# Kernel optimization log

Measured on AMD Instinct MI355X. Metric: run time of the kernel, lower is better.

The kernel has to match this reference:

```python
import jax, jax.numpy as jnp
import numpy as np

# dims: B=32 batch, F=40 max_frames, NB=36 num_boxes, R=512 region size, H=512 hidden
# feat_size D = R + 2H = 1536 ; relation attn input = 2D = 3072

def _soft_attention(feats, hidden, Wf, bf, Wh, bh, wa):
    # feats: (N, L, Din), hidden: (N, H) -> att feat (N, Din), alpha (N, L)
    e = jnp.tanh(feats @ Wf.T + bf + (hidden @ Wh.T + bh)[:, None, :]) @ wa  # (N, L)
    alpha = jax.nn.softmax(e, axis=1)
    att = jnp.einsum('nl,nld->nd', alpha, feats)
    return att, alpha


def setup_inputs() -> dict:
    key = jax.random.key(0)
    ks = jax.random.split(key, 16)
    B, F, NB, R, H = 32, 40, 36, 512, 512
    D = R + 2 * H  # 1536
    s = 0.02
    inp = {
        'i3d_feats': jax.random.normal(ks[0], (B, F, 2 * H), jnp.float32),
        'object_feats': jax.random.normal(ks[1], (B, F, NB, R), jnp.float32),
        'hidden_state': jax.random.normal(ks[2], (B, H), jnp.float32),
        # spatial SoftAttention(R, H, H)
        'Ws_f': jax.random.normal(ks[3], (H, R), jnp.float32) * s,
        'bs_f': jnp.zeros((H,), jnp.float32),
        'Ws_h': jax.random.normal(ks[4], (H, H), jnp.float32) * s,
        'bs_h': jnp.zeros((H,), jnp.float32),
        'was': jax.random.normal(ks[5], (H,), jnp.float32) * s,
        # relation SoftAttention(2D, H, H)
        'Wr_f': jax.random.normal(ks[6], (H, 2 * D), jnp.float32) * s,
        'br_f': jnp.zeros((H,), jnp.float32),
        'Wr_h': jax.random.normal(ks[7], (H, H), jnp.float32) * s,
        'br_h': jnp.zeros((H,), jnp.float32),
        'war': jax.random.normal(ks[8], (H,), jnp.float32) * s,
    }
    return inp


def reference(i3d_feats, object_feats, hidden_state,
              Ws_f, bs_f, Ws_h, bs_h, was,
              Wr_f, br_f, Wr_h, br_h, war):
    B, F, NB, R = object_feats.shape
    # ---- spatial attention over boxes (per frame) ----
    feats = object_feats.reshape(B * F, NB, R)
    hidden_rep = jnp.repeat(hidden_state, F, axis=0)  # == hidden.repeat(1,F).reshape(B*F,-1)
    obj_att, _ = _soft_attention(feats, hidden_rep, Ws_f, bs_f, Ws_h, bs_h, was)
    obj_att = obj_att.reshape(B, F, R)
    feat = jnp.concatenate([obj_att, i3d_feats], axis=-1)  # (B, F, D)
    D = feat.shape[-1]
    # ---- relation attention over all F*F frame pairs ----
    # pairwise[b, i*F + j] = concat(feat[b, j], feat[b, i])  (feat1 varies fast, feat2 slow)
    # Decompose Wr_f @ concat(fj, fi) = Wr1 @ fj + Wr2 @ fi to avoid O(F^2 * 2D) tensor.
    Wr1, Wr2 = Wr_f[:, :D], Wr_f[:, D:]
    p1 = feat @ Wr1.T  # (B, F, H), applied to fast index j
    p2 = feat @ Wr2.T  # (B, F, H), applied to slow index i
    hproj = hidden_state @ Wr_h.T + br_h  # (B, H)
    e = jnp.tanh(p2[:, :, None, :] + p1[:, None, :, :] + (hproj + br_f)[:, None, None, :]) @ war  # (B,F,F) [i,j]
    alpha = jax.nn.softmax(e.reshape(B, F * F), axis=1).reshape(B, F, F)
    # weighted sum of concat(feat[j], feat[i]) splits into two marginal sums
    rel1 = jnp.einsum('bij,bjd->bd', alpha, feat)
    rel2 = jnp.einsum('bij,bid->bd', alpha, feat)
    return jnp.concatenate([rel1, rel2], axis=-1)  # (B, 2D)
```

## Files before the change

kernel.cpp:

```cpp
#include <hip/hip_runtime.h>
#include <stdint.h>

#define B_SZ 32
#define F_SZ 40
#define NB_SZ 36
#define R_SZ 512
#define H_SZ 512
#define D_SZ 1536
#define M1 (B_SZ * F_SZ * NB_SZ)
#define NROW (B_SZ * F_SZ)
#define FNB (F_SZ * NB_SZ)

typedef __attribute__((ext_vector_type(8))) short short8;
typedef __attribute__((ext_vector_type(4))) float f32x4;

__device__ __forceinline__ unsigned short f2bf(float f) {
    unsigned int x = __float_as_uint(f);
    return (unsigned short)((x + 0x7fffu + ((x >> 16) & 1u)) >> 16);
}
__device__ __forceinline__ float bf2f(unsigned short u) {
    union { unsigned int i; float f; } v; v.i = ((unsigned int)u) << 16; return v.f;
}
__device__ __forceinline__ unsigned int cvtpk(float lo, float hi) {
    unsigned int r;
    asm("v_cvt_pk_bf16_f32 %0, %1, %2" : "=v"(r) : "v"(lo), "v"(hi));
    return r;
}
__device__ __forceinline__ float fast_rcp(float x) {
    float r; asm("v_rcp_f32 %0, %1" : "=v"(r) : "v"(x)); return r;
}
__device__ __forceinline__ float fast_tanh(float x) {
    float t = __builtin_amdgcn_exp2f(2.8853900817779268f * x);
    return 1.0f - 2.0f * fast_rcp(t + 1.0f);
}

__device__ __forceinline__ void gload_lds16(const void* gsrc, void* ldst) {
    __builtin_amdgcn_global_load_lds(
        (const __attribute__((address_space(1))) unsigned int*)gsrc,
        (__attribute__((address_space(3))) unsigned int*)ldst, 16, 0, 0);
}

__global__ __launch_bounds__(256) void k_pre(
    const float* __restrict__ hidden,
    const float* __restrict__ Wsh, const float* __restrict__ bsh,
    const float* __restrict__ bsf,
    const float* __restrict__ Wrh, const float* __restrict__ brh,
    const float* __restrict__ brf,
    float* __restrict__ hs, float* __restrict__ hr,
    const float* __restrict__ Wsf, unsigned short* __restrict__ Wsb)
{
    const int t = threadIdx.x;
    if (blockIdx.x >= 256) {
        int i = ((blockIdx.x - 256) * 256 + t) * 8;
        float4 f0 = *(const float4*)(Wsf + i);
        float4 f1 = *(const float4*)(Wsf + i + 4);
        uint4 pk = {cvtpk(f0.x, f0.y), cvtpk(f0.z, f0.w),
                    cvtpk(f1.x, f1.y), cvtpk(f1.z, f1.w)};
        *(uint4*)(Wsb + i) = pk;
        return;
    }
    __shared__ float hid[H_SZ];
    const int b = blockIdx.x >> 3, hc = blockIdx.x & 7;
    for (int i = t; i < H_SZ; i += 256) hid[i] = hidden[b * H_SZ + i];
    __syncthreads();
    const int h = hc * 64 + (t >> 2), kq = t & 3;
    const float* r1 = Wsh + (size_t)h * H_SZ + kq * 128;
    const float* r2 = Wrh + (size_t)h * H_SZ + kq * 128;
    const float* hh = hid + kq * 128;
    float a1 = 0.f, a2 = 0.f;
    for (int k = 0; k < 128; k += 4) {
        float4 v1 = *(const float4*)(r1 + k);
        float4 v2 = *(const float4*)(r2 + k);
        a1 += hh[k] * v1.x + hh[k+1] * v1.y + hh[k+2] * v1.z + hh[k+3] * v1.w;
        a2 += hh[k] * v2.x + hh[k+1] * v2.y + hh[k+2] * v2.z + hh[k+3] * v2.w;
    }
    a1 += __shfl_xor(a1, 1); a1 += __shfl_xor(a1, 2);
    a2 += __shfl_xor(a2, 1); a2 += __shfl_xor(a2, 2);
    if (kq == 0) {
        hs[b * H_SZ + h] = a1 + bsh[h] + bsf[h];
        hr[b * H_SZ + h] = a2 + brh[h] + brf[h];
    }
}

__global__ __launch_bounds__(256, 3) void k_e1_mfma(
    const float* __restrict__ feats,
    const unsigned short* __restrict__ Wsb,
    const float* __restrict__ was,
    const float* __restrict__ hs,
    float* __restrict__ e1p)
{
    __shared__ __align__(16) unsigned char As[2][64 * 128];
    __shared__ __align__(16) unsigned char Bs[2][128 * 128];
    __shared__ float hsl[2][256];
    __shared__ float wasl[256];
    __shared__ float eps[2][64];

    const int bx = blockIdx.x;
    const int wid = (bx & 7) * 180 + (bx >> 3);
    const int mb = wid >> 1, by = wid & 1;
    const int m0 = mb * 64, hb = by * 256;
    const int t = threadIdx.x;
    const int b0 = m0 / FNB, b1 = (m0 + 63) / FNB;
    const int thr = (b0 + 1) * FNB - m0;

    hsl[0][t] = hs[b0 * H_SZ + hb + t];
    hsl[1][t] = hs[b1 * H_SZ + hb + t];
    wasl[t]   = was[hb + t];

    const int lane = t & 63, w = t >> 6;
    const int wr = w >> 1, wc = w & 1;
    const int l15 = lane & 15, lk = lane >> 4;

    int ar[2], brw[4];
#pragma unroll
    for (int i = 0; i < 2; i++) ar[i] = wr * 32 + i * 16 + l15;
#pragma unroll
    for (int j = 0; j < 4; j++) brw[j] = wc * 64 + j * 16 + l15;

    const int srow = t >> 3;
    const int scol = t & 7;
    const int wub  = (t & 192) * 16;

    float4 alo[2], ahi[2];
    f32x4 acc[2][8] = {};
    float ep[2][4] = {{0.f}};

#define E1_LOAD_A(K0) do { \
    _Pragma("unroll") \
    for (int it = 0; it < 2; it++) { \
        int cid = it * 256 + t; \
        int r = cid >> 3, c = cid & 7; \
        const float* src = feats + (size_t)(m0 + r) * R_SZ + (K0) + c * 8; \
        alo[it] = *(const float4*)src; \
        ahi[it] = *(const float4*)(src + 4); \
    } } while (0)

#define E1_WRITE_A(AB) do { \
    _Pragma("unroll") \
    for (int it = 0; it < 2; it++) { \
        int cid = it * 256 + t; \
        int r = cid >> 3, c = cid & 7; \
        uint4 pk = {cvtpk(alo[it].x, alo[it].y), cvtpk(alo[it].z, alo[it].w), \
                    cvtpk(ahi[it].x, ahi[it].y), cvtpk(ahi[it].z, ahi[it].w)}; \
        *(uint4*)(&As[AB][r * 128 + ((c ^ (r & 7)) << 4)]) = pk; \
    } } while (0)

#define E1_STAGE_B(BUF, HP, K0) do { \
    _Pragma("unroll") \
    for (int it = 0; it < 4; it++) { \
        int r = it * 32 + srow; \
        int gc = scol ^ (r & 7); \
        gload_lds16(Wsb + (size_t)(hb + (HP) * 128 + r) * R_SZ + (K0) + gc * 8, \
                    &Bs[BUF][it * 4096 + wub]); \
    } } while (0)

#define E1_COMPUTE(HP, BB, AB) do { \
    __builtin_amdgcn_s_setprio(1); \
    _Pragma("unroll") \
    for (int ks = 0; ks < 2; ks++) { \
        short8 a[2], bv[4]; \
        int c = ks * 4 + lk; \
        _Pragma("unroll") \
        for (int i = 0; i < 2; i++) \
            a[i] = *(const short8*)(&As[AB][ar[i] * 128 + ((c ^ (ar[i] & 7)) << 4)]); \
        _Pragma("unroll") \
        for (int j = 0; j < 4; j++) \
            bv[j] = *(const short8*)(&Bs[BB][brw[j] * 128 + ((c ^ (brw[j] & 7)) << 4)]); \
        _Pragma("unroll") \
        for (int i = 0; i < 2; i++) \
        _Pragma("unroll") \
        for (int j = 0; j < 4; j++) \
            acc[i][(HP) * 4 + j] = __builtin_amdgcn_mfma_f32_16x16x32_bf16( \
                a[i], bv[j], acc[i][(HP) * 4 + j], 0, 0, 0); \
    } \
    __builtin_amdgcn_s_setprio(0); \
    } while (0)

    E1_LOAD_A(0);
    E1_STAGE_B(0, 0, 0);
    E1_WRITE_A(0);
    asm volatile("s_waitcnt vmcnt(0) lgkmcnt(0)\ns_barrier" ::: "memory");

#pragma unroll
    for (int ki = 0; ki < 8; ki++) {
        const int ab = ki & 1;
        E1_STAGE_B(1, 1, ki * 64);
        if (ki < 7) E1_LOAD_A((ki + 1) * 64);
        E1_COMPUTE(0, 0, ab);
        if (ki < 7) {
            asm volatile("s_waitcnt vmcnt(4)\ns_barrier" ::: "memory");
        } else {
            asm volatile("s_waitcnt vmcnt(0)\ns_barrier" ::: "memory");
        }
        if (ki < 7) E1_STAGE_B(0, 0, (ki + 1) * 64);
        E1_COMPUTE(1, 1, ab);
        if (ki < 7) E1_WRITE_A(ab ^ 1);
        asm volatile("s_waitcnt vmcnt(0) lgkmcnt(0)\ns_barrier" ::: "memory");
    }

#pragma unroll
    for (int jj = 0; jj < 8; jj++) {
        int hl = (jj >> 2) * 128 + wc * 64 + (jj & 3) * 16 + l15;
        float wv = wasl[hl];
#pragma unroll
        for (int i = 0; i < 2; i++) {
#pragma unroll
            for (int q = 0; q < 4; q++) {
                int r = wr * 32 + i * 16 + lk * 4 + q;
                float hv = hsl[r >= thr ? 1 : 0][hl];
                ep[i][q] += fast_tanh(acc[i][jj][q] + hv) * wv;
            }
        }
    }
#pragma unroll
    for (int i = 0; i < 2; i++)
#pragma unroll
        for (int q = 0; q < 4; q++) {
            float v = ep[i][q];
            v += __shfl_xor(v, 1);
            v += __shfl_xor(v, 2);
            v += __shfl_xor(v, 4);
            v += __shfl_xor(v, 8);
            if (l15 == 0) eps[wc][wr * 32 + i * 16 + lk * 4 + q] = v;
        }
    __syncthreads();
    if (t < 64) e1p[(size_t)by * M1 + m0 + t] = eps[0][t] + eps[1][t];
#undef E1_LOAD_A
#undef E1_WRITE_A
#undef E1_STAGE_B
#undef E1_COMPUTE
}

__global__ __launch_bounds__(256) void k_softatt(
    const float* __restrict__ feats,
    const float* __restrict__ i3d,
    const float* __restrict__ e1p,
    unsigned short* __restrict__ feat)
{
    __shared__ float alpha[2][NB_SZ];
    const int n0 = blockIdx.x * 2;
    const int t = threadIdx.x;
    const int w = t >> 6;

    if (w < 2) {
        const int n = n0 + w, lane = t & 63;
        float v = -1e30f;
        if (lane < NB_SZ) {
            int idx = n * NB_SZ + lane;
            v = e1p[idx] + e1p[M1 + idx];
        }
        float m = v;
#pragma unroll
        for (int off = 32; off; off >>= 1) m = fmaxf(m, __shfl_xor(m, off));
        float ex = (lane < NB_SZ) ? __expf(v - m) : 0.f;
        float ssum = ex;
#pragma unroll
        for (int off = 32; off; off >>= 1) ssum += __shfl_xor(ssum, off);
        if (lane < NB_SZ) alpha[w][lane] = ex / ssum;
    }
    __syncthreads();

    const int g = t >> 7, lc = t & 127;
    const int n = n0 + g;
    float4 a4 = {0.f, 0.f, 0.f, 0.f};
    const float* base = feats + (size_t)n * NB_SZ * R_SZ + lc * 4;
    for (int ll = 0; ll < NB_SZ; ll++) {
        float al = alpha[g][ll];
        float4 pv = *(const float4*)(base + ll * R_SZ);
        a4.x += al * pv.x; a4.y += al * pv.y;
        a4.z += al * pv.z; a4.w += al * pv.w;
    }
    uint2 att = {cvtpk(a4.x, a4.y), cvtpk(a4.z, a4.w)};
    *(uint2*)(feat + (size_t)n * D_SZ + lc * 4) = att;

    const float* ib = i3d + (size_t)n * 1024 + lc * 8;
    float4 iv0 = *(const float4*)ib;
    float4 iv1 = *(const float4*)(ib + 4);
    uint4 pk = {cvtpk(iv0.x, iv0.y), cvtpk(iv0.z, iv0.w),
                cvtpk(iv1.x, iv1.y), cvtpk(iv1.z, iv1.w)};
    *(uint4*)(feat + (size_t)n * D_SZ + 512 + lc * 8) = pk;
}

__global__ __launch_bounds__(256) void k_pgemm_mfma(
    const unsigned short* __restrict__ feat,
    const float* __restrict__ Wrf,
    float* __restrict__ p)
{
    __shared__ __align__(16) unsigned char As[2][64 * 256];
    __shared__ __align__(16) unsigned char Bs[2][32 * 256];

    const int bx = blockIdx.x;
    const int wid = (bx & 7) * 80 + (bx >> 3);
    const int mb = wid % 20, nb = wid / 20;
    const int m0 = mb * 64, j0 = nb * 32;
    const int t = threadIdx.x;

    const int lane = t & 63, w = t >> 6;
    const int wrm = w >> 1, wcn = w & 1;
    const int l15 = lane & 15, lk = lane >> 4;

    int arow[2];
    arow[0] = wrm * 32 + l15; arow[1] = arow[0] + 16;
    const int brow = wcn * 16 + l15;

    const size_t brow_base = (j0 < 512) ? (size_t)j0 * 3072
                                        : ((size_t)(j0 - 512) * 3072 + 1536);

    float4 blo[2], bhi[2];
    f32x4 acc[2] = {};

#define PG_STAGE_A(BUF, K0) do { \
    _Pragma("unroll") \
    for (int it = 0; it < 4; it++) { \
        int cid = it * 256 + t; \
        int r = cid >> 4, c = cid & 15; \
        int gc = c ^ (r & 7); \
        gload_lds16(feat + (size_t)(m0 + r) * D_SZ + (K0) + gc * 8, \
                    &As[BUF][it * 4096 + (t & 192) * 16]); \
    } } while (0)

#define PG_LOAD_B(K0) do { \
    _Pragma("unroll") \
    for (int it = 0; it < 2; it++) { \
        int cid = it * 256 + t; \
        int r = cid >> 4, c = cid & 15; \
        const float* src = Wrf + brow_base + (size_t)r * 3072 + (K0) + c * 8; \
        blo[it] = *(const float4*)src; \
        bhi[it] = *(const float4*)(src + 4); \
    } } while (0)

#define PG_WRITE_B(BUF) do { \
    _Pragma("unroll") \
    for (int it = 0; it < 2; it++) { \
        int cid = it * 256 + t; \
        int r = cid >> 4, c = cid & 15; \
        uint4 pk = {cvtpk(blo[it].x, blo[it].y), cvtpk(blo[it].z, blo[it].w), \
                    cvtpk(bhi[it].x, bhi[it].y), cvtpk(bhi[it].z, bhi[it].w)}; \
        *(uint4*)(&Bs[BUF][r * 256 + ((c ^ (r & 7)) << 4)]) = pk; \
    } } while (0)

#define PG_COMPUTE(BUF) do { \
    __builtin_amdgcn_s_setprio(1); \
    _Pragma("unroll") \
    for (int ks = 0; ks < 4; ks++) { \
        int c = ks * 4 + lk; \
        short8 a0 = *(const short8*)(&As[BUF][arow[0] * 256 + ((c ^ (arow[0] & 7)) << 4)]); \
        short8 a1 = *(const short8*)(&As[BUF][arow[1] * 256 + ((c ^ (arow[1] & 7)) << 4)]); \
        short8 bv = *(const short8*)(&Bs[BUF][brow * 256 + ((c ^ (brow & 7)) << 4)]); \
        acc[0] = __builtin_amdgcn_mfma_f32_16x16x32_bf16(a0, bv, acc[0], 0, 0, 0); \
        acc[1] = __builtin_amdgcn_mfma_f32_16x16x32_bf16(a1, bv, acc[1], 0, 0, 0); \
    } \
    __builtin_amdgcn_s_setprio(0); \
    } while (0)

    PG_LOAD_B(0);
    PG_STAGE_A(0, 0);
    PG_WRITE_B(0);
    __syncthreads();

#pragma unroll
    for (int ki = 0; ki < 12; ki++) {
        const int cur = ki & 1;
        if (ki < 11) {
            PG_LOAD_B((ki + 1) * 128);
            PG_STAGE_A(cur ^ 1, (ki + 1) * 128);
        }
        PG_COMPUTE(cur);
        if (ki < 11) PG_WRITE_B(cur ^ 1);
        __syncthreads();
    }

#pragma unroll
    for (int i = 0; i < 2; i++)
#pragma unroll
        for (int q = 0; q < 4; q++) {
            int row = m0 + wrm * 32 + i * 16 + lk * 4 + q;
            int col = j0 + wcn * 16 + l15;
            p[(size_t)row * 1024 + col] = acc[i][q];
        }
#undef PG_STAGE_A
#undef PG_LOAD_B
#undef PG_WRITE_B
#undef PG_COMPUTE
}

__global__ __launch_bounds__(256) void k_e2(
    const float* __restrict__ p,
    const float* __restrict__ hr,
    const float* __restrict__ war,
    float* __restrict__ e2)
{
    __shared__ float p1l[F_SZ][512];
    const int blk = blockIdx.x;
    const int b = blk / 10, io = blk % 10;
    const int t = threadIdx.x;
    const int w = t >> 6, l = t & 63;

#pragma unroll
    for (int u = 0; u < 10; u++) {
        int cid = u * 256 + t;
        int r = cid >> 6, c = cid & 63;
        const float* src = p + (size_t)(b * F_SZ + r) * 1024 + c * 8;
        *(float4*)&p1l[r][c * 8]     = *(const float4*)src;
        *(float4*)&p1l[r][c * 8 + 4] = *(const float4*)(src + 4);
    }

    const int i = io * 4 + w;
    const int ni = b * F_SZ + i;
    float base[8], warf[8];
    {
        float4 pa = *(const float4*)(p + (size_t)ni * 1024 + 512 + l * 8);
        float4 pb = *(const float4*)(p + (size_t)ni * 1024 + 512 + l * 8 + 4);
        float4 ha = *(const float4*)(hr + b * H_SZ + l * 8);
        float4 hb = *(const float4*)(hr + b * H_SZ + l * 8 + 4);
        base[0] = pa.x + ha.x; base[1] = pa.y + ha.y; base[2] = pa.z + ha.z; base[3] = pa.w + ha.w;
        base[4] = pb.x + hb.x; base[5] = pb.y + hb.y; base[6] = pb.z + hb.z; base[7] = pb.w + hb.w;
        float4 wa = *(const float4*)(war + l * 8);
        float4 wb = *(const float4*)(war + l * 8 + 4);
        warf[0] = wa.x; warf[1] = wa.y; warf[2] = wa.z; warf[3] = wa.w;
        warf[4] = wb.x; warf[5] = wb.y; warf[6] = wb.z; warf[7] = wb.w;
    }
    __syncthreads();

    for (int j = 0; j < F_SZ; j++) {
        const float* r = p1l[j];
        float4 va = *(const float4*)(r + l * 8);
        float4 vb = *(const float4*)(r + l * 8 + 4);
        float pv[8] = {va.x, va.y, va.z, va.w, vb.x, vb.y, vb.z, vb.w};
        float s = 0.f;
#pragma unroll
        for (int u = 0; u < 8; u++) s += fast_tanh(pv[u] + base[u]) * warf[u];
#pragma unroll
        for (int off = 32; off; off >>= 1) s += __shfl_xor(s, off);
        if (l == 0) e2[(size_t)b * 1600 + i * F_SZ + j] = s;
    }
}

__global__ __launch_bounds__(256) void k_out(
    const float* __restrict__ e2,
    const unsigned short* __restrict__ feat,
    float* __restrict__ out)
{
    __shared__ float alpha[1600];
    __shared__ float red[4];
    __shared__ float rs[F_SZ], cs[F_SZ];
    const int b = blockIdx.x / 6, sx = blockIdx.x % 6;
    const int t = threadIdx.x;
    const int w = t >> 6, l = t & 63;

    float lm = -1e30f;
    for (int idx = t; idx < 1600; idx += 256) {
        float v = e2[(size_t)b * 1600 + idx];
        alpha[idx] = v;
        lm = fmaxf(lm, v);
    }
#pragma unroll
    for (int off = 32; off; off >>= 1) lm = fmaxf(lm, __shfl_xor(lm, off));
    if (l == 0) red[w] = lm;
    __syncthreads();
    float M = fmaxf(fmaxf(red[0], red[1]), fmaxf(red[2], red[3]));
    __syncthreads();
    float ls = 0.f;
    for (int idx = t; idx < 1600; idx += 256) {
        float ex = __expf(alpha[idx] - M);
        alpha[idx] = ex;
        ls += ex;
    }
#pragma unroll
    for (int off = 32; off; off >>= 1) ls += __shfl_xor(ls, off);
    if (l == 0) red[w] = ls;
    __syncthreads();
    float inv = 1.f / (red[0] + red[1] + red[2] + red[3]);

    if (t < F_SZ) {
        float s = 0.f;
        for (int j = 0; j < F_SZ; j++) s += alpha[t * F_SZ + j];
        rs[t] = s * inv;
    } else if (t >= 128 && t < 128 + F_SZ) {
        int j = t - 128;
        float s = 0.f;
        for (int i2 = 0; i2 < F_SZ; i2++) s += alpha[i2 * F_SZ + j];
        cs[j] = s * inv;
    }
    __syncthreads();

    const int cb = sx * 256;
    float a1 = 0.f, a2 = 0.f;
    for (int r = 0; r < F_SZ; r++) {
        float w1 = cs[r], w2 = rs[r];
        float f = bf2f(feat[(size_t)(b * F_SZ + r) * D_SZ + cb + t]);
        a1 += w1 * f;
        a2 += w2 * f;
    }
    out[(size_t)b * 3072 + cb + t]        = a1;
    out[(size_t)b * 3072 + 1536 + cb + t] = a2;
}

extern "C" void kernel_launch(void* const* d_in, const int* in_sizes, int n_in,
                              void* d_out, int out_size, void* d_ws, size_t ws_size,
                              hipStream_t stream) {
    const float* i3d    = (const float*)d_in[0];
    const float* objf   = (const float*)d_in[1];
    const float* hidden = (const float*)d_in[2];
    const float* Wsf    = (const float*)d_in[3];
    const float* bsf    = (const float*)d_in[4];
    const float* Wsh    = (const float*)d_in[5];
    const float* bsh    = (const float*)d_in[6];
    const float* was    = (const float*)d_in[7];
    const float* Wrf    = (const float*)d_in[8];
    const float* brf    = (const float*)d_in[9];
    const float* Wrh    = (const float*)d_in[10];
    const float* brh    = (const float*)d_in[11];
    const float* war    = (const float*)d_in[12];
    float* out = (float*)d_out;

    char* ws = (char*)d_ws;
    float* hs  = (float*)(ws);
    float* hr  = (float*)(ws + 65536);
    float* p   = (float*)(ws + 131072);
    float* e1p = (float*)(ws + 131072);
    unsigned short* Wsb = (unsigned short*)(ws + 4849664);
    float* e2  = (float*)(ws + 5373952);
    unsigned short* feat = (unsigned short*)(ws + 5578752);

    k_pre<<<dim3(384), dim3(256), 0, stream>>>(hidden, Wsh, bsh, bsf, Wrh, brh, brf, hs, hr, Wsf, Wsb);
    k_e1_mfma<<<dim3(1440), dim3(256), 0, stream>>>(objf, Wsb, was, hs, e1p);
    k_softatt<<<dim3(640), dim3(256), 0, stream>>>(objf, i3d, e1p, feat);
    k_pgemm_mfma<<<dim3(640), dim3(256), 0, stream>>>(feat, Wrf, p);
    k_e2<<<dim3(320), dim3(256), 0, stream>>>(p, hr, war, e2);
    k_out<<<dim3(192), dim3(256), 0, stream>>>(e2, feat, out);
}
```

Measured before the change: 262.9 us.

## Split e1 launch in two, drop setprio and custom waitcnt barriers, reshape e2

```diff
diff --git a/kernel.cpp b/kernel.cpp
--- a/kernel.cpp
+++ b/kernel.cpp
@@ -87,7 +87,8 @@
     const unsigned short* __restrict__ Wsb,
     const float* __restrict__ was,
     const float* __restrict__ hs,
-    float* __restrict__ e1p)
+    float* __restrict__ e1p,
+    int wbase)
 {
     __shared__ __align__(16) unsigned char As[2][64 * 128];
     __shared__ __align__(16) unsigned char Bs[2][128 * 128];
@@ -96,7 +97,7 @@
     __shared__ float eps[2][64];
 
     const int bx = blockIdx.x;
-    const int wid = (bx & 7) * 180 + (bx >> 3);
+    const int wid = wbase + (bx & 7) * 90 + (bx >> 3);
     const int mb = wid >> 1, by = wid & 1;
     const int m0 = mb * 64, hb = by * 256;
     const int t = threadIdx.x;
@@ -155,7 +156,6 @@
     } } while (0)
 
 #define E1_COMPUTE(HP, BB, AB) do { \
-    __builtin_amdgcn_s_setprio(1); \
     _Pragma("unroll") \
     for (int ks = 0; ks < 2; ks++) { \
         short8 a[2], bv[4]; \
@@ -172,30 +172,23 @@
         for (int j = 0; j < 4; j++) \
             acc[i][(HP) * 4 + j] = __builtin_amdgcn_mfma_f32_16x16x32_bf16( \
                 a[i], bv[j], acc[i][(HP) * 4 + j], 0, 0, 0); \
-    } \
-    __builtin_amdgcn_s_setprio(0); \
-    } while (0)
+    } } while (0)
 
     E1_LOAD_A(0);
     E1_STAGE_B(0, 0, 0);
     E1_WRITE_A(0);
-    asm volatile("s_waitcnt vmcnt(0) lgkmcnt(0)\ns_barrier" ::: "memory");
-
-#pragma unroll
+    __syncthreads();
+
     for (int ki = 0; ki < 8; ki++) {
         const int ab = ki & 1;
         E1_STAGE_B(1, 1, ki * 64);
         if (ki < 7) E1_LOAD_A((ki + 1) * 64);
         E1_COMPUTE(0, 0, ab);
-        if (ki < 7) {
-            asm volatile("s_waitcnt vmcnt(4)\ns_barrier" ::: "memory");
-        } else {
-            asm volatile("s_waitcnt vmcnt(0)\ns_barrier" ::: "memory");
-        }
+        __syncthreads();
         if (ki < 7) E1_STAGE_B(0, 0, (ki + 1) * 64);
         E1_COMPUTE(1, 1, ab);
         if (ki < 7) E1_WRITE_A(ab ^ 1);
-        asm volatile("s_waitcnt vmcnt(0) lgkmcnt(0)\ns_barrier" ::: "memory");
+        __syncthreads();
     }
 
 #pragma unroll
@@ -340,7 +333,6 @@
     } } while (0)
 
 #define PG_COMPUTE(BUF) do { \
-    __builtin_amdgcn_s_setprio(1); \
     _Pragma("unroll") \
     for (int ks = 0; ks < 4; ks++) { \
         int c = ks * 4 + lk; \
@@ -349,9 +341,7 @@
         short8 bv = *(const short8*)(&Bs[BUF][brow * 256 + ((c ^ (brow & 7)) << 4)]); \
         acc[0] = __builtin_amdgcn_mfma_f32_16x16x32_bf16(a0, bv, acc[0], 0, 0, 0); \
         acc[1] = __builtin_amdgcn_mfma_f32_16x16x32_bf16(a1, bv, acc[1], 0, 0, 0); \
-    } \
-    __builtin_amdgcn_s_setprio(0); \
-    } while (0)
+    } } while (0)
 
     PG_LOAD_B(0);
     PG_STAGE_A(0, 0);
@@ -384,28 +374,27 @@
 #undef PG_COMPUTE
 }
 
-__global__ __launch_bounds__(256) void k_e2(
+__global__ __launch_bounds__(320) void k_e2(
     const float* __restrict__ p,
     const float* __restrict__ hr,
     const float* __restrict__ war,
     float* __restrict__ e2)
 {
     __shared__ float p1l[F_SZ][512];
-    const int blk = blockIdx.x;
-    const int b = blk / 10, io = blk % 10;
+    const int b = blockIdx.x >> 3, io = blockIdx.x & 7;
     const int t = threadIdx.x;
     const int w = t >> 6, l = t & 63;
 
 #pragma unroll
-    for (int u = 0; u < 10; u++) {
-        int cid = u * 256 + t;
+    for (int u = 0; u < 8; u++) {
+        int cid = u * 320 + t;
         int r = cid >> 6, c = cid & 63;
         const float* src = p + (size_t)(b * F_SZ + r) * 1024 + c * 8;
         *(float4*)&p1l[r][c * 8]     = *(const float4*)src;
         *(float4*)&p1l[r][c * 8 + 4] = *(const float4*)(src + 4);
     }
 
-    const int i = io * 4 + w;
+    const int i = io * 5 + w;
     const int ni = b * F_SZ + i;
     float base[8], warf[8];
     {
@@ -524,9 +513,10 @@
     unsigned short* feat = (unsigned short*)(ws + 5578752);
 
     k_pre<<<dim3(384), dim3(256), 0, stream>>>(hidden, Wsh, bsh, bsf, Wrh, brh, brf, hs, hr, Wsf, Wsb);
-    k_e1_mfma<<<dim3(1440), dim3(256), 0, stream>>>(objf, Wsb, was, hs, e1p);
+    k_e1_mfma<<<dim3(720), dim3(256), 0, stream>>>(objf, Wsb, was, hs, e1p, 0);
+    k_e1_mfma<<<dim3(720), dim3(256), 0, stream>>>(objf, Wsb, was, hs, e1p, 720);
     k_softatt<<<dim3(640), dim3(256), 0, stream>>>(objf, i3d, e1p, feat);
     k_pgemm_mfma<<<dim3(640), dim3(256), 0, stream>>>(feat, Wrf, p);
-    k_e2<<<dim3(320), dim3(256), 0, stream>>>(p, hr, war, e2);
+    k_e2<<<dim3(256), dim3(320), 0, stream>>>(p, hr, war, e2);
     k_out<<<dim3(192), dim3(256), 0, stream>>>(e2, feat, out);
 }
```

New measurement: 267.9 us. No clear change (+1.9%).
